# Optimization experiments

Measured on AMD Instinct MI355X. Metric: run time of the kernel, lower is better.

## Reference

```python
import jax, jax.numpy as jnp
import numpy as np

B, S, HID = 2, 2048, 1024
NH, HD = 16, 64
EPS = 1e-12


def setup_inputs() -> dict:
    key = jax.random.key(0)
    ks = jax.random.split(key, 6)
    w_scale = 1.0 / np.sqrt(HID)
    return {
        "hidden_states": jax.random.normal(ks[0], (B, S, HID), dtype=jnp.float32),
        "attention_mask": jnp.ones((B, S), dtype=jnp.float32),
        "Wq": jax.random.normal(ks[1], (HID, HID), dtype=jnp.float32) * w_scale,
        "bq": jnp.zeros((HID,), dtype=jnp.float32),
        "Wk": jax.random.normal(ks[2], (HID, HID), dtype=jnp.float32) * w_scale,
        "bk": jnp.zeros((HID,), dtype=jnp.float32),
        "Wv": jax.random.normal(ks[3], (HID, HID), dtype=jnp.float32) * w_scale,
        "bv": jnp.zeros((HID,), dtype=jnp.float32),
        "Wd": jax.random.normal(ks[4], (HID, HID), dtype=jnp.float32) * w_scale,
        "bd": jnp.zeros((HID,), dtype=jnp.float32),
        "ln_gamma": jnp.ones((HID,), dtype=jnp.float32),
        "ln_beta": jnp.zeros((HID,), dtype=jnp.float32),
    }


def _heads(x):  # [B,S,HID] -> [B,NH,S,HD]
    return x.reshape(B, S, NH, HD).transpose(0, 2, 1, 3)


def reference(hidden_states, attention_mask, Wq, bq, Wk, bk, Wv, bv, Wd, bd, ln_gamma, ln_beta):
    # pre-LayerNorm
    mu = jnp.mean(hidden_states, axis=-1, keepdims=True)
    var = jnp.mean(jnp.square(hidden_states - mu), axis=-1, keepdims=True)
    h = (hidden_states - mu) * jax.lax.rsqrt(var + EPS) * ln_gamma + ln_beta

    q = _heads(h @ Wq.T + bq)  # [B,NH,S,HD]
    k = _heads(h @ Wk.T + bk)
    v = _heads(h @ Wv.T + bv)

    # additive mask: -1000 * (1 - mask), broadcast over heads and query pos
    add_mask = -1000.0 * (1.0 - attention_mask)[:, None, None, :]  # [B,1,1,S]

    # scale applied symmetrically to q and k: sqrt(sqrt(HD)) each
    scale = np.sqrt(np.sqrt(HD)).astype(np.float32)
    scores = jnp.einsum("bhqd,bhkd->bhqk", q / scale, k / scale) + add_mask
    probs = jax.nn.softmax(scores, axis=-1)  # dropout p=0 -> identity
    ctx = jnp.einsum("bhqk,bhkd->bhqd", probs, v)  # [B,NH,S,HD]

    ctx = ctx.transpose(0, 2, 1, 3).reshape(B, S, HID)
    return ctx @ Wd.T + bd
```

## Files before the change

### kernel.cpp

```cpp
#include <hip/hip_runtime.h>
#include <hip/hip_bf16.h>
#include <math.h>

#define BATCH 2
#define SEQ   2048
#define HID   1024
#define NH    16
#define HD    64
#define MROWS (BATCH * SEQ)
#define VSTR  4160

typedef unsigned short u16;
typedef short bf16x8 __attribute__((ext_vector_type(8)));
typedef short bf16x4 __attribute__((ext_vector_type(4)));
typedef float f32x4  __attribute__((ext_vector_type(4)));

#define LOG2E 1.4426950408889634f
#define C2    (0.125f * LOG2E)
#define M2F   23.083120f

static __device__ __forceinline__ u16 f2bf(float f) {
    union { float f; unsigned int u; } v; v.f = f;
    unsigned int r = (v.u + 0x7FFF + ((v.u >> 16) & 1)) >> 16;
    return (u16)r;
}

static __device__ __forceinline__ unsigned int pk_bf16(float a, float b) {
    union { __hip_bfloat162 h; unsigned int u; } r;
    float2 f; f.x = a; f.y = b;
    r.h = __float22bfloat162_rn(f);
    return r.u;
}

static __device__ __forceinline__ f32x4 mfma16(bf16x8 a, bf16x8 b, f32x4 c) {
    return __builtin_amdgcn_mfma_f32_16x16x32_bf16(a, b, c, 0, 0, 0);
}

static __device__ __forceinline__ f32x4 mfma16k16(bf16x4 a, bf16x4 b, f32x4 c) {
#if __has_builtin(__builtin_amdgcn_mfma_f32_16x16x16bf16_1k)
    return __builtin_amdgcn_mfma_f32_16x16x16bf16_1k(a, b, c, 0, 0, 0);
#else
    bf16x8 a8 = {a[0], a[1], a[2], a[3], 0, 0, 0, 0};
    bf16x8 b8 = {b[0], b[1], b[2], b[3], 0, 0, 0, 0};
    return __builtin_amdgcn_mfma_f32_16x16x32_bf16(a8, b8, c, 0, 0, 0);
#endif
}

static __device__ __forceinline__ void ldsload16(const void* g, void* l) {
    __builtin_amdgcn_global_load_lds(
        (const __attribute__((address_space(1))) void*)(unsigned long long)(uintptr_t)g,
        (__attribute__((address_space(3))) void*)(unsigned int)(uintptr_t)l,
        16, 0, 0);
}

__global__ __launch_bounds__(256) void prep_kernel(const float* __restrict__ x,
                                                   const float* __restrict__ gamma,
                                                   const float* __restrict__ beta,
                                                   u16* __restrict__ h,
                                                   const float* __restrict__ w0,
                                                   const float* __restrict__ w1,
                                                   const float* __restrict__ w2,
                                                   const float* __restrict__ w3,
                                                   u16* o0, u16* o1, u16* o2, u16* o3,
                                                   const float* __restrict__ maskg,
                                                   float* __restrict__ m2g)
{
    __shared__ float red[8];
    const int t = threadIdx.x;
    if (blockIdx.x >= 8192) {
        const int idx = ((blockIdx.x - 8192) * 256 + t) * 4;
        const float4 m = *(const float4*)(maskg + idx);
        float4 o;
        o.x = fmaf(-1000.0f * (1.0f - m.x), LOG2E, -M2F);
        o.y = fmaf(-1000.0f * (1.0f - m.y), LOG2E, -M2F);
        o.z = fmaf(-1000.0f * (1.0f - m.z), LOG2E, -M2F);
        o.w = fmaf(-1000.0f * (1.0f - m.w), LOG2E, -M2F);
        *(float4*)(m2g + idx) = o;
        return;
    }
    if (blockIdx.x < 4096) {
        const int blk = blockIdx.x;
        const int which = blk >> 10;
        const int lb = blk & 1023;
        const float* src = which == 0 ? w0 : which == 1 ? w1 : which == 2 ? w2 : w3;
        u16* dst = which == 0 ? o0 : which == 1 ? o1 : which == 2 ? o2 : o3;
        const int idx = (lb * 256 + t) * 4;
        const float4 f = *(const float4*)(src + idx);
        union { u16 s[4]; uint2 v; } p;
        p.s[0] = f2bf(f.x); p.s[1] = f2bf(f.y); p.s[2] = f2bf(f.z); p.s[3] = f2bf(f.w);
        *(uint2*)(dst + idx) = p.v;
        return;
    }
    const int row = blockIdx.x - 4096;
    const float4 xv = ((const float4*)(x + (size_t)row * HID))[t];
    float s  = xv.x + xv.y + xv.z + xv.w;
    float ss = xv.x * xv.x + xv.y * xv.y + xv.z * xv.z + xv.w * xv.w;
#pragma unroll
    for (int off = 32; off > 0; off >>= 1) {
        s  += __shfl_down(s, off);
        ss += __shfl_down(ss, off);
    }
    const int wid = t >> 6;
    if ((t & 63) == 0) { red[wid] = s; red[4 + wid] = ss; }
    __syncthreads();
    s  = red[0] + red[1] + red[2] + red[3];
    ss = red[4] + red[5] + red[6] + red[7];
    const float mu   = s * (1.0f / HID);
    const float var  = ss * (1.0f / HID) - mu * mu;
    const float rstd = rsqrtf(var + 1e-12f);
    const float4 g  = ((const float4*)gamma)[t];
    const float4 bb = ((const float4*)beta)[t];
    union { u16 s[4]; uint2 v; } p;
    p.s[0] = f2bf((xv.x - mu) * rstd * g.x + bb.x);
    p.s[1] = f2bf((xv.y - mu) * rstd * g.y + bb.y);
    p.s[2] = f2bf((xv.z - mu) * rstd * g.z + bb.z);
    p.s[3] = f2bf((xv.w - mu) * rstd * g.w + bb.w);
    ((uint2*)(h + (size_t)row * HID))[t] = p.v;
}

static __device__ __forceinline__ void gemm_core(const u16* __restrict__ A,
                                                 const u16* __restrict__ B,
                                                 int K, int bm, int bn,
                                                 u16* As, u16* Bs,
                                                 int wave, int lane,
                                                 f32x4 acc[4][4])
{
    const int l15  = lane & 15;
    const int quad = lane >> 4;
    const int wm = (wave >> 1) * 64;
    const int wn = (wave & 1) * 64;

    const int c1 = wave * 64 + lane;
    const int c2 = c1 + 256;
    const u16* A1 = A + (size_t)(bm + (c1 >> 2)) * K + (c1 & 3) * 8;
    const u16* A2 = A + (size_t)(bm + (c2 >> 2)) * K + (c2 & 3) * 8;
    const u16* B1 = B + (size_t)(bn + (c1 >> 2)) * K + (c1 & 3) * 8;
    const u16* B2 = B + (size_t)(bn + (c2 >> 2)) * K + (c2 & 3) * 8;
    const int o1 = wave * 512;
    const int o2 = 2048 + wave * 512;

    ldsload16(A1, As + o1);
    ldsload16(A2, As + o2);
    ldsload16(B1, Bs + o1);
    ldsload16(B2, Bs + o2);

    const int nstep = K >> 5;
    for (int i = 0; i < nstep; i++) {
        __syncthreads();
        const int cb = (i & 1) * 4096;
        if (i + 1 < nstep) {
            const int nb = ((i + 1) & 1) * 4096;
            const int k0 = (i + 1) * 32;
            ldsload16(A1 + k0, As + nb + o1);
            ldsload16(A2 + k0, As + nb + o2);
            ldsload16(B1 + k0, Bs + nb + o1);
            ldsload16(B2 + k0, Bs + nb + o2);
        }
        bf16x8 af[4], bfr[4];
#pragma unroll
        for (int mt = 0; mt < 4; mt++)
            af[mt] = *(const bf16x8*)&As[cb + (wm + mt * 16 + l15) * 32 + quad * 8];
#pragma unroll
        for (int nt = 0; nt < 4; nt++)
            bfr[nt] = *(const bf16x8*)&Bs[cb + (wn + nt * 16 + l15) * 32 + quad * 8];
#pragma unroll
        for (int mt = 0; mt < 4; mt++)
#pragma unroll
            for (int nt = 0; nt < 4; nt++)
                acc[mt][nt] = mfma16(af[mt], bfr[nt], acc[mt][nt]);
    }
}

__global__ __launch_bounds__(256) void qkv_gemm(const u16* __restrict__ h,
                                                const u16* __restrict__ wq,
                                                const u16* __restrict__ wk,
                                                const u16* __restrict__ wv,
                                                const float* __restrict__ bq,
                                                const float* __restrict__ bk,
                                                const float* __restrict__ bv,
                                                u16* __restrict__ qo,
                                                u16* __restrict__ ko,
                                                u16* __restrict__ vo)
{
    __shared__ u16 As[8192];
    __shared__ u16 Bs[8192];
    const int blk  = blockIdx.x;
    const int wave = threadIdx.x >> 6;
    const int lane = threadIdx.x & 63;
    const int l15  = lane & 15;
    const int quad = lane >> 4;
    const int wm = (wave >> 1) * 64;
    const int wn = (wave & 1) * 64;

    f32x4 acc[4][4];
#pragma unroll
    for (int mt = 0; mt < 4; mt++)
#pragma unroll
        for (int nt = 0; nt < 4; nt++) acc[mt][nt] = (f32x4)0.0f;

    if (blk < 512) {
        const u16* W     = (blk < 256) ? wq : wk;
        const float* bia = (blk < 256) ? bq : bk;
        u16* out         = (blk < 256) ? qo : ko;
        const int local = blk & 255;
        const int bm = (local >> 3) * 128;
        const int bn = (local & 7) * 128;
        gemm_core(h, W, HID, bm, bn, As, Bs, wave, lane, acc);

        float bv4[4];
#pragma unroll
        for (int nt = 0; nt < 4; nt++) bv4[nt] = bia[bn + wn + nt * 16 + l15];
#pragma unroll
        for (int mt = 0; mt < 4; mt++)
#pragma unroll
            for (int r = 0; r < 4; r++) {
                const int m  = bm + wm + mt * 16 + quad * 4 + r;
                const int bI = m >> 11;
                const int sI = m & (SEQ - 1);
#pragma unroll
                for (int nt = 0; nt < 4; nt++) {
                    const int n  = bn + wn + nt * 16 + l15;
                    const int hh = n >> 6;
                    const int d  = n & 63;
                    out[(((size_t)(bI * NH + hh) * SEQ + sI) << 6) + d] =
                        f2bf(acc[mt][nt][r] + bv4[nt]);
                }
            }
    } else {
        const int local = blk - 512;
        const int bm = (local & 7) * 128;
        const int bn = (local >> 3) * 128;
        gemm_core(wv, h, HID, bm, bn, As, Bs, wave, lane, acc);

#pragma unroll
        for (int mt = 0; mt < 4; mt++) {
            const f32x4 bm4 = *(const f32x4*)&bv[bm + wm + mt * 16 + quad * 4];
#pragma unroll
            for (int r = 0; r < 4; r++) {
                const int row = bm + wm + mt * 16 + quad * 4 + r;
#pragma unroll
                for (int nt = 0; nt < 4; nt++) {
                    const int col = bn + wn + nt * 16 + l15;
                    vo[(size_t)row * VSTR + col] = f2bf(acc[mt][nt][r] + bm4[r]);
                }
            }
        }
    }
}

__global__ __launch_bounds__(256) void out_gemm(const u16* __restrict__ ctx,
                                                const u16* __restrict__ wd,
                                                const float* __restrict__ bd,
                                                float* __restrict__ out)
{
    __shared__ u16 As[8192];
    __shared__ u16 Bs[8192];
    const int blk  = blockIdx.x;
    const int wave = threadIdx.x >> 6;
    const int lane = threadIdx.x & 63;
    const int l15  = lane & 15;
    const int quad = lane >> 4;
    const int wm = (wave >> 1) * 64;
    const int wn = (wave & 1) * 64;
    const int bm = (blk >> 3) * 128;
    const int bn = (blk & 7) * 128;

    f32x4 acc[4][4];
#pragma unroll
    for (int mt = 0; mt < 4; mt++)
#pragma unroll
        for (int nt = 0; nt < 4; nt++) acc[mt][nt] = (f32x4)0.0f;

    gemm_core(ctx, wd, HID, bm, bn, As, Bs, wave, lane, acc);

    float bv4[4];
#pragma unroll
    for (int nt = 0; nt < 4; nt++) bv4[nt] = bd[bn + wn + nt * 16 + l15];
#pragma unroll
    for (int mt = 0; mt < 4; mt++)
#pragma unroll
        for (int r = 0; r < 4; r++) {
            const int m = bm + wm + mt * 16 + quad * 4 + r;
#pragma unroll
            for (int nt = 0; nt < 4; nt++) {
                const int n = bn + wn + nt * 16 + l15;
                out[(size_t)m * HID + n] = acc[mt][nt][r] + bv4[nt];
            }
        }
}

__global__ __launch_bounds__(256) void attn_mfma(const u16* __restrict__ qb,
                                                 const u16* __restrict__ kb,
                                                 const u16* __restrict__ vtb,
                                                 const float* __restrict__ m2g,
                                                 u16* __restrict__ ctx)
{
    __shared__ __align__(16) char smem[34816];

    const int t    = threadIdx.x;
    const int wave = t >> 6;
    const int lane = t & 63;
    const int l15  = lane & 15;
    const int quad = lane >> 4;

    const int bh = blockIdx.x & 31;
    const int qt = blockIdx.x >> 5;
    const int b  = bh >> 4;
    const int hh = bh & 15;
    const int q0 = qt * 128;

    const size_t headoff = (size_t)(b * NH + hh) * SEQ * HD;
    const u16* kbase = kb + headoff;
    const u16* vbase = vtb + (size_t)(hh * HD) * VSTR + b * SEQ;
    const float* m2b = m2g + b * SEQ;

    bf16x8 Qf[2][2];
#pragma unroll
    for (int nt = 0; nt < 2; nt++)
#pragma unroll
        for (int ks2 = 0; ks2 < 2; ks2++)
            Qf[nt][ks2] = *(const bf16x8*)(qb + headoff +
                (size_t)(q0 + wave * 32 + nt * 16 + l15) * HD + ks2 * 32 + quad * 8);

    f32x4 O[4][2];
#pragma unroll
    for (int mt2 = 0; mt2 < 4; mt2++)
#pragma unroll
        for (int nt = 0; nt < 2; nt++) O[mt2][nt] = (f32x4)0.0f;
    float ls2[2] = {0.0f, 0.0f};

    const int srow = lane >> 3;
    const int lcol = (lane & 7) ^ srow;
    const int swk0 = ((quad)     ^ (l15 & 7)) * 8;
    const int swk1 = ((quad + 4) ^ (l15 & 7)) * 8;
    const int g0 = wave * 2;

    ldsload16(kbase + (size_t)(g0 * 8 + srow) * HD + lcol * 8,           smem + g0 * 1024);
    ldsload16(kbase + (size_t)(g0 * 8 + 8 + srow) * HD + lcol * 8,       smem + g0 * 1024 + 1024);
    ldsload16(vbase + (size_t)(g0 * 8 + srow) * VSTR + lcol * 8,         smem + 16384 + g0 * 1024);
    ldsload16(vbase + (size_t)(g0 * 8 + 8 + srow) * VSTR + lcol * 8,     smem + 16384 + g0 * 1024 + 1024);

    for (int i = 0; i < 32; i++) {
        __syncthreads();
        const int c0 = i * 64;
        const u16* Ks  = (const u16*)(smem + (i & 1) * 8192);
        const u16* Vts = (const u16*)(smem + 16384 + (i & 1) * 8192);
        if (i + 1 < 32) {
            const int cn = c0 + 64;
            char* nbK = smem + ((i + 1) & 1) * 8192;
            char* nbV = smem + 16384 + ((i + 1) & 1) * 8192;
            ldsload16(kbase + (size_t)(cn + g0 * 8 + srow) * HD + lcol * 8,       nbK + g0 * 1024);
            ldsload16(kbase + (size_t)(cn + g0 * 8 + 8 + srow) * HD + lcol * 8,   nbK + g0 * 1024 + 1024);
            ldsload16(vbase + (size_t)(g0 * 8 + srow) * VSTR + cn + lcol * 8,     nbV + g0 * 1024);
            ldsload16(vbase + (size_t)(g0 * 8 + 8 + srow) * VSTR + cn + lcol * 8, nbV + g0 * 1024 + 1024);
        }

        bf16x4 Pk[4][2];
#pragma unroll
        for (int ks = 0; ks < 4; ks++) {
            const int rb = (ks * 16 + l15) * 64;
            const bf16x8 ka0 = *(const bf16x8*)&Ks[rb + swk0];
            const bf16x8 ka1 = *(const bf16x8*)&Ks[rb + swk1];
            f32x4 St[2];
#pragma unroll
            for (int nt = 0; nt < 2; nt++) {
                f32x4 a = (f32x4)0.0f;
                a = mfma16(ka0, Qf[nt][0], a);
                a = mfma16(ka1, Qf[nt][1], a);
                St[nt] = a;
            }
            const f32x4 mv = *(const f32x4*)(m2b + c0 + ks * 16 + quad * 4);
#pragma unroll
            for (int nt = 0; nt < 2; nt++) {
                const float p0 = __builtin_amdgcn_exp2f(fmaf(St[nt][0], C2, mv[0]));
                const float p1 = __builtin_amdgcn_exp2f(fmaf(St[nt][1], C2, mv[1]));
                const float p2 = __builtin_amdgcn_exp2f(fmaf(St[nt][2], C2, mv[2]));
                const float p3 = __builtin_amdgcn_exp2f(fmaf(St[nt][3], C2, mv[3]));
                ls2[nt] += (p0 + p1) + (p2 + p3);
                union { unsigned int u[2]; bf16x4 v; } pk;
                pk.u[0] = pk_bf16(p0, p1);
                pk.u[1] = pk_bf16(p2, p3);
                Pk[ks][nt] = pk.v;
            }
        }

#pragma unroll
        for (int mt2 = 0; mt2 < 4; mt2++) {
            const u16* Vp = Vts + (mt2 * 16 + l15) * 64 + ((quad & 1) << 2);
            bf16x4 Va[4];
#pragma unroll
            for (int ks = 0; ks < 4; ks++)
                Va[ks] = *(const bf16x4*)(Vp +
                    ((((ks << 1) | (quad >> 1)) ^ (l15 & 7)) << 3));
#pragma unroll
            for (int nt = 0; nt < 2; nt++) {
                f32x4 acc = O[mt2][nt];
#pragma unroll
                for (int ks = 0; ks < 4; ks++)
                    acc = mfma16k16(Va[ks], Pk[ks][nt], acc);
                O[mt2][nt] = acc;
            }
        }
    }

#pragma unroll
    for (int nt = 0; nt < 2; nt++) {
        ls2[nt] += __shfl_xor(ls2[nt], 16);
        ls2[nt] += __shfl_xor(ls2[nt], 32);
    }
    const float linv0 = 1.0f / ls2[0];
    const float linv1 = 1.0f / ls2[1];

    __syncthreads();
    float* Ot = (float*)smem + wave * (32 * 68);
#pragma unroll
    for (int mt2 = 0; mt2 < 4; mt2++)
#pragma unroll
        for (int nt = 0; nt < 2; nt++) {
            const f32x4 v = O[mt2][nt] * (nt ? linv1 : linv0);
            *(f32x4*)(Ot + (nt * 16 + l15) * 68 + mt2 * 16 + quad * 4) = v;
        }
    {
        const int ql   = lane >> 1;
        const int half = lane & 1;
        const float* srcp = Ot + ql * 68 + half * 32;
        u16* dstp = ctx + (size_t)(b * SEQ + q0 + wave * 32 + ql) * HID
                        + hh * 64 + half * 32;
#pragma unroll
        for (int j = 0; j < 4; j++) {
            union { u16 s[8]; uint4 v; } p;
#pragma unroll
            for (int ii = 0; ii < 8; ii++) p.s[ii] = f2bf(srcp[j * 8 + ii]);
            *(uint4*)(dstp + j * 8) = p.v;
        }
    }
}

extern "C" void kernel_launch(void* const* d_in, const int* in_sizes, int n_in,
                              void* d_out, int out_size, void* d_ws, size_t ws_size,
                              hipStream_t stream)
{
    const float* hs    = (const float*)d_in[0];
    const float* mask  = (const float*)d_in[1];
    const float* Wq    = (const float*)d_in[2];
    const float* bq    = (const float*)d_in[3];
    const float* Wk    = (const float*)d_in[4];
    const float* bk    = (const float*)d_in[5];
    const float* Wv    = (const float*)d_in[6];
    const float* bv    = (const float*)d_in[7];
    const float* Wd    = (const float*)d_in[8];
    const float* bd    = (const float*)d_in[9];
    const float* gamma = (const float*)d_in[10];
    const float* beta  = (const float*)d_in[11];
    float* out = (float*)d_out;

    const size_t NE = (size_t)MROWS * HID;
    u16* ws   = (u16*)d_ws;
    u16* h    = ws;
    u16* qbb  = ws + NE;
    u16* kbb  = qbb + NE;
    u16* vtb  = kbb + NE;
    u16* ctxb = vtb + (size_t)HID * VSTR;
    u16* wqb  = ctxb + NE;
    u16* wkb  = wqb + HID * HID;
    u16* wvb  = wkb + HID * HID;
    u16* wdb  = wvb + HID * HID;
    float* m2 = (float*)(wdb + HID * HID);

    prep_kernel<<<8196, 256, 0, stream>>>(hs, gamma, beta, h,
                                          Wq, Wk, Wv, Wd, wqb, wkb, wvb, wdb,
                                          mask, m2);

    qkv_gemm<<<768, 256, 0, stream>>>(h, wqb, wkb, wvb, bq, bk, bv, qbb, kbb, vtb);

    attn_mfma<<<512, 256, 0, stream>>>(qbb, kbb, vtb, m2, ctxb);

    out_gemm<<<256, 256, 0, stream>>>(ctxb, wdb, bd, out);
}
```

Baseline: 223.9 us.

## Stage QKV epilogue through LDS and halve attention query tile per block

The QKV GEMM epilogue now writes results into a swizzled shared-memory tile and then emits 16-byte coalesced stores for both the Q/K head layout and the transposed V layout, replacing scattered 2-byte global stores. The attention kernel drops from 32 to 16 query rows per wave (64 per block) and launches twice as many blocks, giving more parallelism and fewer registers per wave. In exchange, each K/V tile is loaded from global memory twice as often across blocks, and the GEMM epilogue gains two extra barriers.

```diff
diff --git a/kernel.cpp b/kernel.cpp
--- a/kernel.cpp
+++ b/kernel.cpp
@@ -182,11 +182,13 @@
                                                 u16* __restrict__ ko,
                                                 u16* __restrict__ vo)
 {
-    __shared__ u16 As[8192];
-    __shared__ u16 Bs[8192];
+    __shared__ __align__(16) u16 smemT[16384];
+    u16* As = smemT;
+    u16* Bs = smemT + 8192;
     const int blk  = blockIdx.x;
-    const int wave = threadIdx.x >> 6;
-    const int lane = threadIdx.x & 63;
+    const int t    = threadIdx.x;
+    const int wave = t >> 6;
+    const int lane = t & 63;
     const int l15  = lane & 15;
     const int quad = lane >> 4;
     const int wm = (wave >> 1) * 64;
@@ -210,39 +212,70 @@
         float bv4[4];
 #pragma unroll
         for (int nt = 0; nt < 4; nt++) bv4[nt] = bia[bn + wn + nt * 16 + l15];
+
+        __syncthreads();
 #pragma unroll
         for (int mt = 0; mt < 4; mt++)
 #pragma unroll
             for (int r = 0; r < 4; r++) {
-                const int m  = bm + wm + mt * 16 + quad * 4 + r;
-                const int bI = m >> 11;
-                const int sI = m & (SEQ - 1);
+                const int row = wm + mt * 16 + quad * 4 + r;
 #pragma unroll
                 for (int nt = 0; nt < 4; nt++) {
-                    const int n  = bn + wn + nt * 16 + l15;
-                    const int hh = n >> 6;
-                    const int d  = n & 63;
-                    out[(((size_t)(bI * NH + hh) * SEQ + sI) << 6) + d] =
+                    const int colL = wn + nt * 16 + l15;
+                    smemT[row * 128 + ((((colL >> 3) ^ (row & 7)) << 3) | (colL & 7))] =
                         f2bf(acc[mt][nt][r] + bv4[nt]);
                 }
             }
+        __syncthreads();
+        {
+            const int tr = t & 127;
+            const int nh = t >> 7;
+            const int m  = bm + tr;
+            const int bI = m >> 11;
+            const int sI = m & (SEQ - 1);
+            const int n0 = bn + nh * 64;
+            const int hhd = n0 >> 6;
+            u16* dst = out + (((size_t)(bI * NH + hhd) * SEQ + sI) << 6);
+#pragma unroll
+            for (int j = 0; j < 8; j++) {
+                const int colL = nh * 64 + j * 8;
+                const uint4 v = *(const uint4*)&smemT[tr * 128 +
+                    (((colL >> 3) ^ (tr & 7)) << 3)];
+                *(uint4*)(dst + j * 8) = v;
+            }
+        }
     } else {
         const int local = blk - 512;
         const int bm = (local & 7) * 128;
         const int bn = (local >> 3) * 128;
         gemm_core(wv, h, HID, bm, bn, As, Bs, wave, lane, acc);
 
+        __syncthreads();
 #pragma unroll
         for (int mt = 0; mt < 4; mt++) {
             const f32x4 bm4 = *(const f32x4*)&bv[bm + wm + mt * 16 + quad * 4];
 #pragma unroll
             for (int r = 0; r < 4; r++) {
-                const int row = bm + wm + mt * 16 + quad * 4 + r;
+                const int row = wm + mt * 16 + quad * 4 + r;
 #pragma unroll
                 for (int nt = 0; nt < 4; nt++) {
-                    const int col = bn + wn + nt * 16 + l15;
-                    vo[(size_t)row * VSTR + col] = f2bf(acc[mt][nt][r] + bm4[r]);
+                    const int colL = wn + nt * 16 + l15;
+                    smemT[row * 128 + ((((colL >> 3) ^ (row & 7)) << 3) | (colL & 7))] =
+                        f2bf(acc[mt][nt][r] + bm4[r]);
                 }
+            }
+        }
+        __syncthreads();
+        {
+            const int fr = t & 127;
+            const int th = t >> 7;
+            u16* dst = vo + (size_t)(bm + fr) * VSTR + bn + th * 64;
+#pragma unroll
+            for (int j = 0; j < 8; j++) {
+                const int colL = th * 64 + j * 8;
+                const uint4 v = *(const uint4*)&smemT[fr * 128 +
+                    (((colL >> 3) ^ (fr & 7)) << 3)];
+                *(uint4*)(dst + j * 8) = v;
             }
         }
     }
@@ -295,7 +328,7 @@
                                                  const float* __restrict__ m2g,
                                                  u16* __restrict__ ctx)
 {
-    __shared__ __align__(16) char smem[34816];
+    __shared__ __align__(16) char smem[32768];
 
     const int t    = threadIdx.x;
     const int wave = t >> 6;
@@ -307,27 +340,25 @@
     const int qt = blockIdx.x >> 5;
     const int b  = bh >> 4;
     const int hh = bh & 15;
-    const int q0 = qt * 128;
+    const int q0 = qt * 64;
 
     const size_t headoff = (size_t)(b * NH + hh) * SEQ * HD;
     const u16* kbase = kb + headoff;
     const u16* vbase = vtb + (size_t)(hh * HD) * VSTR + b * SEQ;
     const float* m2b = m2g + b * SEQ;
 
-    bf16x8 Qf[2][2];
-#pragma unroll
-    for (int nt = 0; nt < 2; nt++)
+    bf16x8 Qf[2];
+    {
+        const int qrow = q0 + wave * 16 + l15;
 #pragma unroll
         for (int ks2 = 0; ks2 < 2; ks2++)
-            Qf[nt][ks2] = *(const bf16x8*)(qb + headoff +
-                (size_t)(q0 + wave * 32 + nt * 16 + l15) * HD + ks2 * 32 + quad * 8);
-
-    f32x4 O[4][2];
-#pragma unroll
-    for (int mt2 = 0; mt2 < 4; mt2++)
-#pragma unroll
-        for (int nt = 0; nt < 2; nt++) O[mt2][nt] = (f32x4)0.0f;
-    float ls2[2] = {0.0f, 0.0f};
+            Qf[ks2] = *(const bf16x8*)(qb + headoff + (size_t)qrow * HD + ks2 * 32 + quad * 8);
+    }
+
+    f32x4 O[4];
+#pragma unroll
+    for (int mt2 = 0; mt2 < 4; mt2++) O[mt2] = (f32x4)0.0f;
+    float ls = 0.0f;
 
     const int srow = lane >> 3;
     const int lcol = (lane & 7) ^ srow;
@@ -355,33 +386,25 @@
             ldsload16(vbase + (size_t)(g0 * 8 + 8 + srow) * VSTR + cn + lcol * 8, nbV + g0 * 1024 + 1024);
         }
 
-        bf16x4 Pk[4][2];
+        bf16x4 Pk[4];
 #pragma unroll
         for (int ks = 0; ks < 4; ks++) {
             const int rb = (ks * 16 + l15) * 64;
             const bf16x8 ka0 = *(const bf16x8*)&Ks[rb + swk0];
             const bf16x8 ka1 = *(const bf16x8*)&Ks[rb + swk1];
-            f32x4 St[2];
-#pragma unroll
-            for (int nt = 0; nt < 2; nt++) {
-                f32x4 a = (f32x4)0.0f;
-                a = mfma16(ka0, Qf[nt][0], a);
-                a = mfma16(ka1, Qf[nt][1], a);
-                St[nt] = a;
-            }
+            f32x4 a = (f32x4)0.0f;
+            a = mfma16(ka0, Qf[0], a);
+            a = mfma16(ka1, Qf[1], a);
             const f32x4 mv = *(const f32x4*)(m2b + c0 + ks * 16 + quad * 4);
-#pragma unroll
-            for (int nt = 0; nt < 2; nt++) {
-                const float p0 = __builtin_amdgcn_exp2f(fmaf(St[nt][0], C2, mv[0]));
-                const float p1 = __builtin_amdgcn_exp2f(fmaf(St[nt][1], C2, mv[1]));
-                const float p2 = __builtin_amdgcn_exp2f(fmaf(St[nt][2], C2, mv[2]));
-                const float p3 = __builtin_amdgcn_exp2f(fmaf(St[nt][3], C2, mv[3]));
-                ls2[nt] += (p0 + p1) + (p2 + p3);
-                union { unsigned int u[2]; bf16x4 v; } pk;
-                pk.u[0] = pk_bf16(p0, p1);
-                pk.u[1] = pk_bf16(p2, p3);
-                Pk[ks][nt] = pk.v;
-            }
+            const float p0 = __builtin_amdgcn_exp2f(fmaf(a[0], C2, mv[0]));
+            const float p1 = __builtin_amdgcn_exp2f(fmaf(a[1], C2, mv[1]));
+            const float p2 = __builtin_amdgcn_exp2f(fmaf(a[2], C2, mv[2]));
+            const float p3 = __builtin_amdgcn_exp2f(fmaf(a[3], C2, mv[3]));
+            ls += (p0 + p1) + (p2 + p3);
+            union { unsigned int u[2]; bf16x4 v; } pk;
+            pk.u[0] = pk_bf16(p0, p1);
+            pk.u[1] = pk_bf16(p2, p3);
+            Pk[ks] = pk.v;
         }
 
 #pragma unroll
@@ -392,42 +415,33 @@
             for (int ks = 0; ks < 4; ks++)
                 Va[ks] = *(const bf16x4*)(Vp +
                     ((((ks << 1) | (quad >> 1)) ^ (l15 & 7)) << 3));
-#pragma unroll
-            for (int nt = 0; nt < 2; nt++) {
-                f32x4 acc = O[mt2][nt];
-#pragma unroll
-                for (int ks = 0; ks < 4; ks++)
-                    acc = mfma16k16(Va[ks], Pk[ks][nt], acc);
-                O[mt2][nt] = acc;
-            }
-        }
-    }
-
-#pragma unroll
-    for (int nt = 0; nt < 2; nt++) {
-        ls2[nt] += __shfl_xor(ls2[nt], 16);
-        ls2[nt] += __shfl_xor(ls2[nt], 32);
-    }
-    const float linv0 = 1.0f / ls2[0];
-    const float linv1 = 1.0f / ls2[1];
+            f32x4 acc = O[mt2];
+#pragma unroll
+            for (int ks = 0; ks < 4; ks++)
+                acc = mfma16k16(Va[ks], Pk[ks], acc);
+            O[mt2] = acc;
+        }
+    }
+
+    ls += __shfl_xor(ls, 16);
+    ls += __shfl_xor(ls, 32);
+    const float linv = 1.0f / ls;
 
     __syncthreads();
-    float* Ot = (float*)smem + wave * (32 * 68);
-#pragma unroll
-    for (int mt2 = 0; mt2 < 4; mt2++)
-#pragma unroll
-        for (int nt = 0; nt < 2; nt++) {
-            const f32x4 v = O[mt2][nt] * (nt ? linv1 : linv0);
-            *(f32x4*)(Ot + (nt * 16 + l15) * 68 + mt2 * 16 + quad * 4) = v;
-        }
+    float* Ot = (float*)smem + wave * (16 * 68);
+#pragma unroll
+    for (int mt2 = 0; mt2 < 4; mt2++) {
+        const f32x4 v = O[mt2] * linv;
+        *(f32x4*)(Ot + l15 * 68 + mt2 * 16 + quad * 4) = v;
+    }
     {
-        const int ql   = lane >> 1;
-        const int half = lane & 1;
-        const float* srcp = Ot + ql * 68 + half * 32;
-        u16* dstp = ctx + (size_t)(b * SEQ + q0 + wave * 32 + ql) * HID
-                        + hh * 64 + half * 32;
-#pragma unroll
-        for (int j = 0; j < 4; j++) {
+        const int ql  = lane >> 2;
+        const int seg = lane & 3;
+        const float* srcp = Ot + ql * 68 + seg * 16;
+        u16* dstp = ctx + (size_t)(b * SEQ + q0 + wave * 16 + ql) * HID
+                        + hh * 64 + seg * 16;
+#pragma unroll
+        for (int j = 0; j < 2; j++) {
             union { u16 s[8]; uint4 v; } p;
 #pragma unroll
             for (int ii = 0; ii < 8; ii++) p.s[ii] = f2bf(srcp[j * 8 + ii]);
@@ -473,7 +487,7 @@
 
     qkv_gemm<<<768, 256, 0, stream>>>(h, wqb, wkb, wvb, bq, bk, bv, qbb, kbb, vtb);
 
-    attn_mfma<<<512, 256, 0, stream>>>(qbb, kbb, vtb, m2, ctxb);
+    attn_mfma<<<1024, 256, 0, stream>>>(qbb, kbb, vtb, m2, ctxb);
 
     out_gemm<<<256, 256, 0, stream>>>(ctxb, wdb, bd, out);
 }
```

After: 226.8 us. No clear change (+1.3%).
